# Kernel optimization log

Hardware: AMD Instinct MI355X
Metric: run time of the kernel (lower is better)

The kernel has to match this reference:

```python
import jax, jax.numpy as jnp
import numpy as np

DIM = 4096
N_HEADS = 32
N_KV_HEADS = 8
HEAD_DIM = DIM // N_HEADS  # 128
N_REP = N_HEADS // N_KV_HEADS  # 4
B, S = 1, 2048
ROPE_THETA = 500000.0


def setup_inputs() -> dict:
    key = jax.random.key(0)
    ks = jax.random.split(key, 5)
    sc = 0.02
    x = jax.random.normal(ks[0], (B, S, DIM), jnp.float32)
    wq = jax.random.normal(ks[1], (DIM, N_HEADS * HEAD_DIM), jnp.float32) * sc
    wk = jax.random.normal(ks[2], (DIM, N_KV_HEADS * HEAD_DIM), jnp.float32) * sc
    wv = jax.random.normal(ks[3], (DIM, N_KV_HEADS * HEAD_DIM), jnp.float32) * sc
    wo = jax.random.normal(ks[4], (N_HEADS * HEAD_DIM, DIM), jnp.float32) * sc
    # rotary frequencies: freqs_cis = exp(i * t * theta^(-2j/d)), j in [0, head_dim/2)
    inv_freq = 1.0 / (ROPE_THETA ** (jnp.arange(0, HEAD_DIM, 2, dtype=jnp.float32) / HEAD_DIM))
    t = jnp.arange(S, dtype=jnp.float32)
    ang = jnp.outer(t, inv_freq)  # (S, head_dim/2)
    freqs_cos = jnp.cos(ang)
    freqs_sin = jnp.sin(ang)
    # additive causal mask, broadcastable to (B, H, S, S)
    mask = jnp.where(jnp.triu(jnp.ones((S, S), bool), k=1), -jnp.inf, 0.0).astype(jnp.float32)[None, None]
    return {"x": x, "wq": wq, "wk": wk, "wv": wv, "wo": wo,
            "freqs_cos": freqs_cos, "freqs_sin": freqs_sin, "mask": mask}


def _apply_rotary(t, cos, sin):
    # t: (B, S, n, hd); complex multiply on consecutive pairs (x0,x1),(x2,x3),...
    b, s, n, hd = t.shape
    tr = t.reshape(b, s, n, hd // 2, 2)
    re, im = tr[..., 0], tr[..., 1]
    c = cos[None, :, None, :]
    sn = sin[None, :, None, :]
    out_re = re * c - im * sn
    out_im = re * sn + im * c
    return jnp.stack([out_re, out_im], axis=-1).reshape(b, s, n, hd)


def reference(x, wq, wk, wv, wo, freqs_cos, freqs_sin, mask):
    b, s, _ = x.shape
    xq = (x @ wq).reshape(b, s, N_HEADS, HEAD_DIM)
    xk = (x @ wk).reshape(b, s, N_KV_HEADS, HEAD_DIM)
    xv = (x @ wv).reshape(b, s, N_KV_HEADS, HEAD_DIM)
    xq = _apply_rotary(xq, freqs_cos, freqs_sin)
    xk = _apply_rotary(xk, freqs_cos, freqs_sin)
    # repeat_kv (GQA): expand kv heads to match query heads
    keys = jnp.repeat(xk, N_REP, axis=2)    # (b, s, H, hd)
    values = jnp.repeat(xv, N_REP, axis=2)
    # (b, H, s, hd)
    q = xq.transpose(0, 2, 1, 3)
    k = keys.transpose(0, 2, 1, 3)
    v = values.transpose(0, 2, 1, 3)
    scores = jnp.einsum('bhqd,bhkd->bhqk', q, k) / np.sqrt(HEAD_DIM).astype(np.float32)
    scores = scores + mask
    probs = jax.nn.softmax(scores.astype(jnp.float32), axis=-1).astype(q.dtype)
    out = jnp.einsum('bhqk,bhkd->bhqd', probs, v)
    out = out.transpose(0, 2, 1, 3).reshape(b, s, N_HEADS * HEAD_DIM)
    return out @ wo
```

## Files before the change

### kernel.cpp

```cpp
#include <hip/hip_runtime.h>
#include <cstdint>
#include <cstddef>

typedef _Float16 f16_t;
typedef f16_t f16x8 __attribute__((ext_vector_type(8)));
typedef float  floatx4 __attribute__((ext_vector_type(4)));

#define S_LEN 2048
#define DIM_  4096
#define NH    32
#define NKV   8
#define HD    128
#define KV_DIM (NKV * HD)
#define QLD   (DIM_ + 2 * KV_DIM)

__device__ __forceinline__ float bf16r(float x) {
    uint32_t u = __float_as_uint(x);
    u = (u + 0x7fffu + ((u >> 16) & 1u)) & 0xffff0000u;
    return __uint_as_float(u);
}

__device__ __forceinline__ void gload_lds16(const f16_t* g, f16_t* l) {
    __builtin_amdgcn_global_load_lds(
        (const __attribute__((address_space(1))) void*)g,
        (__attribute__((address_space(3))) void*)l, 16, 0, 0);
}

__global__ void f32_to_f16_kernel(const float* __restrict__ in,
                                  f16_t* __restrict__ out, int n) {
    int i = (blockIdx.x * blockDim.x + threadIdx.x) * 8;
    if (i >= n) return;
    float4 a = *(const float4*)(in + i);
    float4 b = *(const float4*)(in + i + 4);
    f16x8 o;
    o[0] = (f16_t)bf16r(a.x); o[1] = (f16_t)bf16r(a.y);
    o[2] = (f16_t)bf16r(a.z); o[3] = (f16_t)bf16r(a.w);
    o[4] = (f16_t)bf16r(b.x); o[5] = (f16_t)bf16r(b.y);
    o[6] = (f16_t)bf16r(b.z); o[7] = (f16_t)bf16r(b.w);
    *(f16x8*)(out + i) = o;
}

__global__ void transpose_weights_kernel(const float* __restrict__ wq,
                                         const float* __restrict__ wk,
                                         const float* __restrict__ wv,
                                         const float* __restrict__ wo,
                                         f16_t* __restrict__ wqkvT,
                                         f16_t* __restrict__ woT) {
    __shared__ float tile[32][33];
    int bid = blockIdx.x;
    const float* in; f16_t* out; int C;
    if (bid < 16384)      { in = wq; out = wqkvT;                          C = 4096; }
    else if (bid < 20480) { bid -= 16384; in = wk; out = wqkvT + (size_t)4096 * 4096; C = 1024; }
    else if (bid < 24576) { bid -= 20480; in = wv; out = wqkvT + (size_t)5120 * 4096; C = 1024; }
    else                  { bid -= 24576; in = wo; out = woT;              C = 4096; }
    int gpr = C / 32;
    int bx = (bid % gpr) * 32;
    int by = (bid / gpr) * 32;
    int tx = threadIdx.x, ty = threadIdx.y;
#pragma unroll
    for (int i = 0; i < 4; i++) {
        int r = ty + i * 8;
        tile[r][tx] = in[(size_t)(by + r) * C + bx + tx];
    }
    __syncthreads();
#pragma unroll
    for (int i = 0; i < 4; i++) {
        int r = ty + i * 8;
        out[(size_t)(bx + r) * 4096 + by + tx] = (f16_t)bf16r(tile[tx][r]);
    }
}

__global__ void transpose_f16_kernel(const f16_t* __restrict__ in,
                                     f16_t* __restrict__ out,
                                     int ldi, int ldo) {
    __shared__ float tile[32][33];
    int bx = blockIdx.x * 32;
    int by = blockIdx.y * 32;
    int tx = threadIdx.x, ty = threadIdx.y;
#pragma unroll
    for (int i = 0; i < 4; i++) {
        int r = ty + i * 8;
        tile[r][tx] = (float)in[(size_t)(by + r) * ldi + bx + tx];
    }
    __syncthreads();
#pragma unroll
    for (int i = 0; i < 4; i++) {
        int r = ty + i * 8;
        out[(size_t)(bx + r) * ldo + by + tx] = (f16_t)tile[tx][r];
    }
}

__global__ void rope_qk_kernel(f16_t* __restrict__ QKV,
                               const float* __restrict__ fcos,
                               const float* __restrict__ fsin) {
    int c8 = (blockIdx.x * blockDim.x + threadIdx.x) * 8;
    int row = blockIdx.y;
    f16_t* p = QKV + (size_t)row * QLD + c8;
    f16x8 v = *(f16x8*)p;
    const float* cr = fcos + row * 64 + ((c8 & 127) >> 1);
    const float* sr = fsin + row * 64 + ((c8 & 127) >> 1);
    const float sc = (c8 < DIM_) ? 0.08838834764831845f : 1.0f;
#pragma unroll
    for (int u = 0; u < 4; u++) {
        float cc = bf16r(cr[u]), ss = bf16r(sr[u]);
        float re = (float)v[2 * u], im = (float)v[2 * u + 1];
        v[2 * u]     = (f16_t)((re * cc - im * ss) * sc);
        v[2 * u + 1] = (f16_t)((re * ss + im * cc) * sc);
    }
    *(f16x8*)p = v;
}

template <int BM, int BN, typename OutT>
__global__ __launch_bounds__(512) void gemm_pipe_kernel(
        const f16_t* __restrict__ A, const f16_t* __restrict__ BT,
        OutT* __restrict__ C, int M, int N, int K, int nbx) {
    constexpr int BK = 32;
    constexpr int WN = BN / 64;
    constexpr int WM = 8 / WN;
    constexpr int MT = BM / WM / 16;
    constexpr int NT = 4;
    constexpr int ABY = BM * BK * 2;
    constexpr int BBY = BN * BK * 2;
    constexpr int AISS = ABY / 8192;
    constexpr int BISS = BBY / 8192;
    constexpr int LOADS = AISS + BISS;
    constexpr int BUF_EL = (ABY + BBY) / 2;

    __shared__ f16_t lds[3 * BUF_EL];

    const int tid  = threadIdx.x;
    const int lane = tid & 63;
    const int wave = tid >> 6;
    const int quad = lane >> 4;
    const int l16  = lane & 15;
    const int wn = (wave % WN) * 64;
    const int wm = (wave / WN) * (BM / WM);

    const int nwg = gridDim.x;
    const int swz = (blockIdx.x & 7) * (nwg >> 3) + (blockIdx.x >> 3);
    const int m0 = (swz / nbx) * BM;
    const int n0 = (swz % nbx) * BN;

    const f16_t* Arow = A  + (size_t)m0 * K;
    const f16_t* Brow = BT + (size_t)n0 * K;
    const int nt_tiles = K / BK;

    floatx4 acc[MT][NT] = {};

    auto stage = [&](int t, int q) {
        const int k0 = t * BK;
        f16_t* LdA = lds + q * BUF_EL;
#pragma unroll
        for (int j = 0; j < AISS; j++) {
            int Lb  = j * 8192 + tid * 16;
            int row = Lb >> 6;
            int cb  = (Lb & 48) ^ (((Lb >> 7) & 3) << 4);
            gload_lds16(Arow + (size_t)row * K + k0 + (cb >> 1), LdA + (Lb >> 1));
        }
        f16_t* LdB = lds + q * BUF_EL + ABY / 2;
#pragma unroll
        for (int j = 0; j < BISS; j++) {
            int Lb  = j * 8192 + tid * 16;
            int row = Lb >> 6;
            int cb  = (Lb & 48) ^ (((Lb >> 7) & 3) << 4);
            gload_lds16(Brow + (size_t)row * K + k0 + (cb >> 1), LdB + (Lb >> 1));
        }
    };

    stage(0, 0);
    stage(1, 1);
    if constexpr (LOADS == 4) asm volatile("s_waitcnt vmcnt(4)" ::: "memory");
    else                      asm volatile("s_waitcnt vmcnt(3)" ::: "memory");
    __builtin_amdgcn_s_barrier();
    __builtin_amdgcn_sched_barrier(0);

    for (int t = 0; t < nt_tiles; ++t) {
        const int cur = t % 3;
        const bool pre = (t + 2 < nt_tiles);
        if (pre) stage(t + 2, (t + 2) % 3);

        const f16_t* Ab = lds + cur * BUF_EL;
        const f16_t* Bb = Ab + ABY / 2;
        f16x8 af[MT], bf[NT];
#pragma unroll
        for (int mt = 0; mt < MT; mt++) {
            int r  = wm + mt * 16 + l16;
            int cb = (quad * 16) ^ (((r >> 1) & 3) << 4);
            af[mt] = *(const f16x8*)(Ab + r * 32 + (cb >> 1));
        }
#pragma unroll
        for (int nt = 0; nt < NT; nt++) {
            int r  = wn + nt * 16 + l16;
            int cb = (quad * 16) ^ (((r >> 1) & 3) << 4);
            bf[nt] = *(const f16x8*)(Bb + r * 32 + (cb >> 1));
        }
        __builtin_amdgcn_s_setprio(1);
#pragma unroll
        for (int mt = 0; mt < MT; mt++)
#pragma unroll
            for (int nt = 0; nt < NT; nt++)
                acc[mt][nt] = __builtin_amdgcn_mfma_f32_16x16x32_f16(
                    af[mt], bf[nt], acc[mt][nt], 0, 0, 0);
        __builtin_amdgcn_s_setprio(0);
        if (pre) {
            if constexpr (LOADS == 4) asm volatile("s_waitcnt vmcnt(4)" ::: "memory");
            else                      asm volatile("s_waitcnt vmcnt(3)" ::: "memory");
        } else {
            asm volatile("s_waitcnt vmcnt(0)" ::: "memory");
        }
        __builtin_amdgcn_s_barrier();
        __builtin_amdgcn_sched_barrier(0);
    }

#pragma unroll
    for (int mt = 0; mt < MT; mt++)
#pragma unroll
        for (int nt = 0; nt < NT; nt++)
#pragma unroll
            for (int rg = 0; rg < 4; rg++) {
                int row = m0 + wm + mt * 16 + quad * 4 + rg;
                int col = n0 + wn + nt * 16 + l16;
                C[(size_t)row * N + col] = (OutT)acc[mt][nt][rg];
            }
}

__global__ __launch_bounds__(512) void attn_kernel(
        const f16_t* __restrict__ QKV, const f16_t* __restrict__ Vt,
        f16_t* __restrict__ O) {
    constexpr int BK = 64;
    __shared__ f16_t Ks[BK * HD];
    __shared__ f16_t Vs[HD * BK];
    __shared__ f16_t Ps[8][16][72];

    const int tid  = threadIdx.x;
    const int lane = tid & 63;
    const int wave = tid >> 6;
    const int quad = lane >> 4;
    const int l16  = lane & 15;

    const int bid = blockIdx.x;
    const int h   = bid & 31;
    const int g   = bid >> 5;
    const int qt  = (g < 8) ? g : 23 - g;
    const int q0  = qt * 128;
    const int hkv = h >> 2;

    const int qrow = q0 + wave * 16 + l16;
    const f16_t* Qg = QKV + (size_t)qrow * QLD + h * HD;
    f16x8 qf[4];
#pragma unroll
    for (int c = 0; c < 4; c++) qf[c] = *(const f16x8*)(Qg + c * 32 + quad * 8);

    floatx4 o_acc[8] = {};
    floatx4 l_acc = {0.f, 0.f, 0.f, 0.f};
    float m_run[4];
#pragma unroll
    for (int i = 0; i < 4; i++) m_run[i] = -1e30f;

    f16x8 ones;
#pragma unroll
    for (int i = 0; i < 8; i++) ones[i] = (f16_t)1.0f;

    const int q_lo = q0 + wave * 16;
    const int q_hi = q_lo + 15;
    const int ntiles = q0 / BK + 2;

    const int rK = tid >> 4;
    const int cK = (((tid & 15) * 16) ^ ((rK & 7) << 4)) >> 1;
    const f16_t* pK = QKV + (size_t)rK * QLD + DIM_ + hkv * HD + cK;
    const int rV = tid >> 3;
    const int cV = (((tid & 7) * 16) ^ ((rV & 7) << 4)) >> 1;
    const f16_t* pV = Vt + (size_t)hkv * HD * S_LEN + (size_t)rV * S_LEN + cV;
    f16_t* KsD0 = Ks + tid * 8;  f16_t* KsD1 = KsD0 + 4096;
    f16_t* VsD0 = Vs + tid * 8;  f16_t* VsD1 = VsD0 + 4096;

    for (int t = 0; t < ntiles; t++) {
        const int k0 = t * BK;

        gload_lds16(pK + (size_t)k0 * QLD, KsD0);
        gload_lds16(pK + (size_t)(k0 + 32) * QLD, KsD1);
        gload_lds16(pV + k0, VsD0);
        gload_lds16(pV + k0 + (size_t)64 * S_LEN, VsD1);
        asm volatile("s_waitcnt vmcnt(0)" ::: "memory");
        __syncthreads();

        if (k0 <= q_hi) {
            floatx4 sc4[4] = {};
#pragma unroll
            for (int nt = 0; nt < 4; nt++) {
                const int r = nt * 16 + l16;
#pragma unroll
                for (int ks = 0; ks < 4; ks++) {
                    int cb = (ks * 64 + quad * 16) ^ ((r & 7) << 4);
                    f16x8 kf = *(const f16x8*)(Ks + r * 128 + (cb >> 1));
                    sc4[nt] = __builtin_amdgcn_mfma_f32_16x16x32_f16(qf[ks], kf, sc4[nt], 0, 0, 0);
                }
            }

            if ((k0 + BK - 1) > q_lo) {
#pragma unroll
                for (int nt = 0; nt < 4; nt++)
#pragma unroll
                    for (int rg = 0; rg < 4; rg++) {
                        int qg = q_lo + quad * 4 + rg;
                        int kg = k0 + nt * 16 + l16;
                        if (kg > qg) sc4[nt][rg] = -1e30f;
                    }
            }

            float m_t[4];
#pragma unroll
            for (int rg = 0; rg < 4; rg++) {
                float m = fmaxf(fmaxf(sc4[0][rg], sc4[1][rg]), fmaxf(sc4[2][rg], sc4[3][rg]));
#pragma unroll
                for (int off = 8; off >= 1; off >>= 1)
                    m = fmaxf(m, __shfl_xor(m, off, 64));
                m_t[rg] = m;
            }
            int grow = (m_t[0] > m_run[0] + 8.f) | (m_t[1] > m_run[1] + 8.f) |
                       (m_t[2] > m_run[2] + 8.f) | (m_t[3] > m_run[3] + 8.f);
            if (__any(grow)) {
                float alpha[4];
#pragma unroll
                for (int rg = 0; rg < 4; rg++) {
                    float mn = fmaxf(m_run[rg], m_t[rg]);
                    alpha[rg] = __expf(m_run[rg] - mn);
                    m_run[rg] = mn;
                }
#pragma unroll
                for (int dt = 0; dt < 8; dt++)
#pragma unroll
                    for (int rg = 0; rg < 4; rg++) o_acc[dt][rg] *= alpha[rg];
#pragma unroll
                for (int rg = 0; rg < 4; rg++) l_acc[rg] *= alpha[rg];
            }

#pragma unroll
            for (int nt = 0; nt < 4; nt++)
#pragma unroll
                for (int rg = 0; rg < 4; rg++)
                    Ps[wave][quad * 4 + rg][nt * 16 + l16] =
                        (f16_t)__expf(sc4[nt][rg] - m_run[rg]);
            asm volatile("s_waitcnt lgkmcnt(0)" ::: "memory");
            __builtin_amdgcn_sched_barrier(0);

#pragma unroll
            for (int ks = 0; ks < 2; ks++) {
                f16x8 pf = *(const f16x8*)&Ps[wave][l16][ks * 32 + quad * 8];
                l_acc = __builtin_amdgcn_mfma_f32_16x16x32_f16(pf, ones, l_acc, 0, 0, 0);
#pragma unroll
                for (int dt = 0; dt < 8; dt++) {
                    const int r = dt * 16 + l16;
                    int cb = (ks * 64 + quad * 16) ^ ((r & 7) << 4);
                    f16x8 vf = *(const f16x8*)(Vs + r * 64 + (cb >> 1));
                    o_acc[dt] = __builtin_amdgcn_mfma_f32_16x16x32_f16(pf, vf, o_acc[dt], 0, 0, 0);
                }
            }
        }
        __syncthreads();
    }

#pragma unroll
    for (int rg = 0; rg < 4; rg++) {
        float inv_l = 1.0f / l_acc[rg];
#pragma unroll
        for (int dt = 0; dt < 8; dt++) {
            int row = q0 + wave * 16 + quad * 4 + rg;
            int col = h * HD + dt * 16 + l16;
            O[(size_t)row * (NH * HD) + col] = (f16_t)(o_acc[dt][rg] * inv_l);
        }
    }
}

extern "C" void kernel_launch(void* const* d_in, const int* in_sizes, int n_in,
                              void* d_out, int out_size, void* d_ws, size_t ws_size,
                              hipStream_t stream) {
    const float* x    = (const float*)d_in[0];
    const float* wq   = (const float*)d_in[1];
    const float* wk   = (const float*)d_in[2];
    const float* wv   = (const float*)d_in[3];
    const float* wo   = (const float*)d_in[4];
    const float* fcos = (const float*)d_in[5];
    const float* fsin = (const float*)d_in[6];
    float* out = (float*)d_out;

    char* ws = (char*)d_ws;
    constexpr size_t MB = 1024 * 1024;
    f16_t* xb    = (f16_t*)(ws + 0 * MB);
    f16_t* wqkvT = (f16_t*)(ws + 16 * MB);
    f16_t* woT   = (f16_t*)(ws + 64 * MB);
    f16_t* QKVb  = (f16_t*)(ws + 96 * MB);
    f16_t* Vt    = (f16_t*)(ws + 120 * MB);
    f16_t* attnb = (f16_t*)(ws + 124 * MB);

    f32_to_f16_kernel<<<S_LEN * DIM_ / 8 / 256, 256, 0, stream>>>(x, xb, S_LEN * DIM_);
    transpose_weights_kernel<<<40960, dim3(32, 8), 0, stream>>>(wq, wk, wv, wo, wqkvT, woT);

    gemm_pipe_kernel<256, 256, f16_t><<<192, 512, 0, stream>>>(
        xb, wqkvT, QKVb, S_LEN, QLD, DIM_, QLD / 256);

    rope_qk_kernel<<<dim3(5, S_LEN), 128, 0, stream>>>(QKVb, fcos, fsin);
    transpose_f16_kernel<<<dim3(KV_DIM / 32, S_LEN / 32), dim3(32, 8), 0, stream>>>(
        QKVb + 5120, Vt, QLD, S_LEN);

    attn_kernel<<<512, 512, 0, stream>>>(QKVb, Vt, attnb);

    gemm_pipe_kernel<256, 128, float><<<256, 512, 0, stream>>>(
        attnb, woT, out, S_LEN, DIM_, DIM_, DIM_ / 128);
}
```

Baseline: 507.1 us.

## Restructure GEMM into BK=64 double-buffered 8-phase schedule with 2x2 wave tiling

Replaces the triple-buffered BK=32 GEMM with a double-buffered BK=64 kernel that splits each K-tile into four phases, interleaving LDS fragment loads, barriers and MFMA bursts so that global-to-LDS prefetch of the next tile overlaps compute. Source and destination addresses are precomputed once, a new XOR swizzle is applied for the 64-wide rows, and waves are laid out as a 2x4 grid over two halves of A and B. The output projection switches to a 128x256 tile. The change adds many more barriers per tile and doubles the LDS per buffer, and it sets launch_bounds occupancy to 2, which may pressure registers and LDS.

```diff
diff --git a/kernel.cpp b/kernel.cpp
--- a/kernel.cpp
+++ b/kernel.cpp
@@ -111,106 +111,129 @@
 }
 
 template <int BM, int BN, typename OutT>
-__global__ __launch_bounds__(512) void gemm_pipe_kernel(
+__global__ __launch_bounds__(512, 2) void gemm_8p_kernel(
         const f16_t* __restrict__ A, const f16_t* __restrict__ BT,
         OutT* __restrict__ C, int M, int N, int K, int nbx) {
-    constexpr int BK = 32;
-    constexpr int WN = BN / 64;
-    constexpr int WM = 8 / WN;
-    constexpr int MT = BM / WM / 16;
-    constexpr int NT = 4;
-    constexpr int ABY = BM * BK * 2;
-    constexpr int BBY = BN * BK * 2;
-    constexpr int AISS = ABY / 8192;
-    constexpr int BISS = BBY / 8192;
-    constexpr int LOADS = AISS + BISS;
-    constexpr int BUF_EL = (ABY + BBY) / 2;
-
-    __shared__ f16_t lds[3 * BUF_EL];
+    constexpr int BK = 64;
+    constexpr int MT = BM / 32;
+    constexpr int NT = BN / 64;
+    constexpr int MH = MT / 2;
+    constexpr int AHALF = (BM / 2) * 64;
+    constexpr int BHALF = (BN / 2) * 64;
+    constexpr int BUF   = (BM + BN) * 64;
+    constexpr int AJ = BM / 128;
+    constexpr int BJ = BN / 128;
+
+    __shared__ f16_t lds[2 * BUF];
 
     const int tid  = threadIdx.x;
     const int lane = tid & 63;
     const int wave = tid >> 6;
     const int quad = lane >> 4;
     const int l16  = lane & 15;
-    const int wn = (wave % WN) * 64;
-    const int wm = (wave / WN) * (BM / WM);
+    const int wmi  = wave >> 2;
+    const int wni  = wave & 3;
 
     const int nwg = gridDim.x;
     const int swz = (blockIdx.x & 7) * (nwg >> 3) + (blockIdx.x >> 3);
     const int m0 = (swz / nbx) * BM;
     const int n0 = (swz % nbx) * BN;
 
-    const f16_t* Arow = A  + (size_t)m0 * K;
-    const f16_t* Brow = BT + (size_t)n0 * K;
-    const int nt_tiles = K / BK;
+    const f16_t* srcA[2][AJ]; int dA[2][AJ];
+    const f16_t* srcB[2][BJ]; int dB[2][BJ];
+#pragma unroll
+    for (int h = 0; h < 2; h++)
+#pragma unroll
+        for (int j = 0; j < AJ; j++) {
+            int L = j * 8192 + tid * 16;
+            int r = L >> 7;
+            int c = ((L & 127) ^ (((L >> 9) & 1) << 5)) >> 1;
+            srcA[h][j] = A + (size_t)(m0 + h * (BM / 2) + r) * K + c;
+            dA[h][j] = h * AHALF + (L >> 1);
+        }
+#pragma unroll
+    for (int h = 0; h < 2; h++)
+#pragma unroll
+        for (int j = 0; j < BJ; j++) {
+            int L = j * 8192 + tid * 16;
+            int r = L >> 7;
+            int c = ((L & 127) ^ (((L >> 9) & 1) << 5)) >> 1;
+            srcB[h][j] = BT + (size_t)(n0 + h * (BN / 2) + r) * K + c;
+            dB[h][j] = 2 * AHALF + h * BHALF + (L >> 1);
+        }
+
+    auto stage_all = [&](int tt) {
+        f16_t* base = lds + (tt & 1) * BUF;
+        const int k0 = tt * BK;
+#pragma unroll
+        for (int h = 0; h < 2; h++)
+#pragma unroll
+            for (int j = 0; j < AJ; j++)
+                gload_lds16(srcA[h][j] + k0, base + dA[h][j]);
+#pragma unroll
+        for (int h = 0; h < 2; h++)
+#pragma unroll
+            for (int j = 0; j < BJ; j++)
+                gload_lds16(srcB[h][j] + k0, base + dB[h][j]);
+    };
 
     floatx4 acc[MT][NT] = {};
-
-    auto stage = [&](int t, int q) {
-        const int k0 = t * BK;
-        f16_t* LdA = lds + q * BUF_EL;
-#pragma unroll
-        for (int j = 0; j < AISS; j++) {
-            int Lb  = j * 8192 + tid * 16;
-            int row = Lb >> 6;
-            int cb  = (Lb & 48) ^ (((Lb >> 7) & 3) << 4);
-            gload_lds16(Arow + (size_t)row * K + k0 + (cb >> 1), LdA + (Lb >> 1));
-        }
-        f16_t* LdB = lds + q * BUF_EL + ABY / 2;
-#pragma unroll
-        for (int j = 0; j < BISS; j++) {
-            int Lb  = j * 8192 + tid * 16;
-            int row = Lb >> 6;
-            int cb  = (Lb & 48) ^ (((Lb >> 7) & 3) << 4);
-            gload_lds16(Brow + (size_t)row * K + k0 + (cb >> 1), LdB + (Lb >> 1));
-        }
-    };
-
-    stage(0, 0);
-    stage(1, 1);
-    if constexpr (LOADS == 4) asm volatile("s_waitcnt vmcnt(4)" ::: "memory");
-    else                      asm volatile("s_waitcnt vmcnt(3)" ::: "memory");
+    const int ntk = K / BK;
+
+    stage_all(0);
+    asm volatile("s_waitcnt vmcnt(0)" ::: "memory");
     __builtin_amdgcn_s_barrier();
     __builtin_amdgcn_sched_barrier(0);
 
-    for (int t = 0; t < nt_tiles; ++t) {
-        const int cur = t % 3;
-        const bool pre = (t + 2 < nt_tiles);
-        if (pre) stage(t + 2, (t + 2) % 3);
-
-        const f16_t* Ab = lds + cur * BUF_EL;
-        const f16_t* Bb = Ab + ABY / 2;
-        f16x8 af[MT], bf[NT];
-#pragma unroll
-        for (int mt = 0; mt < MT; mt++) {
-            int r  = wm + mt * 16 + l16;
-            int cb = (quad * 16) ^ (((r >> 1) & 3) << 4);
-            af[mt] = *(const f16x8*)(Ab + r * 32 + (cb >> 1));
-        }
-#pragma unroll
-        for (int nt = 0; nt < NT; nt++) {
-            int r  = wn + nt * 16 + l16;
-            int cb = (quad * 16) ^ (((r >> 1) & 3) << 4);
-            bf[nt] = *(const f16x8*)(Bb + r * 32 + (cb >> 1));
-        }
-        __builtin_amdgcn_s_setprio(1);
-#pragma unroll
-        for (int mt = 0; mt < MT; mt++)
-#pragma unroll
-            for (int nt = 0; nt < NT; nt++)
-                acc[mt][nt] = __builtin_amdgcn_mfma_f32_16x16x32_f16(
-                    af[mt], bf[nt], acc[mt][nt], 0, 0, 0);
-        __builtin_amdgcn_s_setprio(0);
-        if (pre) {
-            if constexpr (LOADS == 4) asm volatile("s_waitcnt vmcnt(4)" ::: "memory");
-            else                      asm volatile("s_waitcnt vmcnt(3)" ::: "memory");
-        } else {
-            asm volatile("s_waitcnt vmcnt(0)" ::: "memory");
-        }
-        __builtin_amdgcn_s_barrier();
-        __builtin_amdgcn_sched_barrier(0);
-    }
+#define PHASE(mh, ks, STAGE, DRAIN)                                           \
+    {                                                                         \
+        STAGE                                                                 \
+        _Pragma("unroll")                                                     \
+        for (int i = 0; i < MH; i++) {                                        \
+            int r_ = ((mh) * MH + i) * 16 + l16;                              \
+            int cb_ = (((ks) * 64) + quad * 16) ^ (((r_ >> 2) & 1) << 5);     \
+            af[i] = *(const f16x8*)(Ab + r_ * 64 + (cb_ >> 1));               \
+        }                                                                     \
+        if ((mh) == 0) {                                                      \
+            _Pragma("unroll")                                                 \
+            for (int nt = 0; nt < NT; nt++) {                                 \
+                int rb_ = (wni & 1) * 64 + nt * 16 + l16;                     \
+                int cb_ = (((ks) * 64) + quad * 16) ^ (((rb_ >> 2) & 1) << 5);\
+                bf[nt] = *(const f16x8*)(Bb + rb_ * 64 + (cb_ >> 1));         \
+            }                                                                 \
+        }                                                                     \
+        __builtin_amdgcn_sched_barrier(0);                                    \
+        __builtin_amdgcn_s_barrier();                                         \
+        asm volatile("s_waitcnt lgkmcnt(0)" ::: "memory");                    \
+        __builtin_amdgcn_sched_barrier(0);                                    \
+        __builtin_amdgcn_s_setprio(1);                                        \
+        _Pragma("unroll")                                                     \
+        for (int i = 0; i < MH; i++)                                          \
+            _Pragma("unroll")                                                 \
+            for (int nt = 0; nt < NT; nt++)                                   \
+                acc[(mh) * MH + i][nt] =                                      \
+                    __builtin_amdgcn_mfma_f32_16x16x32_f16(                   \
+                        af[i], bf[nt], acc[(mh) * MH + i][nt], 0, 0, 0);      \
+        __builtin_amdgcn_s_setprio(0);                                        \
+        DRAIN                                                                 \
+        __builtin_amdgcn_sched_barrier(0);                                    \
+        __builtin_amdgcn_s_barrier();                                         \
+        __builtin_amdgcn_sched_barrier(0);                                    \
+    }
+
+    for (int t = 0; t < ntk; ++t) {
+        const f16_t* Ab = lds + (t & 1) * BUF + wmi * AHALF;
+        const f16_t* Bb = lds + (t & 1) * BUF + 2 * AHALF + (wni >> 1) * BHALF;
+        const bool pre = (t + 1 < ntk);
+        f16x8 af[MH], bf[NT];
+
+        PHASE(0, 0, if (pre) stage_all(t + 1);, )
+        PHASE(1, 0, , )
+        PHASE(0, 1, , )
+        PHASE(1, 1, ,
+              if (pre) { asm volatile("s_waitcnt vmcnt(0)" ::: "memory"); })
+    }
+#undef PHASE
 
 #pragma unroll
     for (int mt = 0; mt < MT; mt++)
@@ -218,8 +241,8 @@
         for (int nt = 0; nt < NT; nt++)
 #pragma unroll
             for (int rg = 0; rg < 4; rg++) {
-                int row = m0 + wm + mt * 16 + quad * 4 + rg;
-                int col = n0 + wn + nt * 16 + l16;
+                int row = m0 + wmi * (BM / 2) + mt * 16 + quad * 4 + rg;
+                int col = n0 + wni * 64 + nt * 16 + l16;
                 C[(size_t)row * N + col] = (OutT)acc[mt][nt][rg];
             }
 }
@@ -396,7 +419,7 @@
     f32_to_f16_kernel<<<S_LEN * DIM_ / 8 / 256, 256, 0, stream>>>(x, xb, S_LEN * DIM_);
     transpose_weights_kernel<<<40960, dim3(32, 8), 0, stream>>>(wq, wk, wv, wo, wqkvT, woT);
 
-    gemm_pipe_kernel<256, 256, f16_t><<<192, 512, 0, stream>>>(
+    gemm_8p_kernel<256, 256, f16_t><<<192, 512, 0, stream>>>(
         xb, wqkvT, QKVb, S_LEN, QLD, DIM_, QLD / 256);
 
     rope_qk_kernel<<<dim3(5, S_LEN), 128, 0, stream>>>(QKVb, fcos, fsin);
@@ -405,6 +428,6 @@
 
     attn_kernel<<<512, 512, 0, stream>>>(QKVb, Vt, attnb);
 
-    gemm_pipe_kernel<256, 128, float><<<256, 512, 0, stream>>>(
-        attnb, woT, out, S_LEN, DIM_, DIM_, DIM_ / 128);
-}
+    gemm_8p_kernel<128, 256, float><<<256, 512, 0, stream>>>(
+        attnb, woT, out, S_LEN, DIM_, DIM_, DIM_ / 256);
+}
```

Result: slower. 529.6 us (+4.4%).
